# Performance work log

Hardware: AMD Instinct MI355X
Metric: run time of the kernel (lower is better)

Reference implementation:

```python
import jax, jax.numpy as jnp
import numpy as np

B, LQ, LK = 8, 64, 256
E, H, D, NH = 128, 4, 32, 128  # embed_time, num_heads, input_dim, nhidden
EK = E // H


def setup_inputs() -> dict:
    key = jax.random.key(0)
    ks = jax.random.split(key, 10)
    s = 1.0 / np.sqrt(E)
    so = 1.0 / np.sqrt(D * H)
    return {
        "query": jax.random.normal(ks[0], (B, LQ, E), jnp.float32),
        "key": jax.random.normal(ks[1], (B, LK, E), jnp.float32),
        "value": jax.random.normal(ks[2], (B, LK, D), jnp.float32),
        "mask": jax.random.randint(ks[3], (B, LK, D), 0, 2, jnp.int32),
        "Wq": jax.random.uniform(ks[4], (E, E), jnp.float32, -s, s),
        "bq": jax.random.uniform(ks[5], (E,), jnp.float32, -s, s),
        "Wk": jax.random.uniform(ks[6], (E, E), jnp.float32, -s, s),
        "bk": jax.random.uniform(ks[7], (E,), jnp.float32, -s, s),
        "Wo": jax.random.uniform(ks[8], (D * H, NH), jnp.float32, -so, so),
        "bo": jax.random.uniform(ks[9], (NH,), jnp.float32, -so, so),
    }


def reference(query, key, value, mask, Wq, bq, Wk, bk, Wo, bo):
    # project and split heads: [B, L, E] -> [B, H, L, EK]
    q = (query @ Wq + bq).reshape(B, LQ, H, EK).transpose(0, 2, 1, 3)
    k = (key @ Wk + bk).reshape(B, LK, H, EK).transpose(0, 2, 1, 3)
    # scores: [B, H, LQ, LK]
    scores = jnp.einsum("bhqe,bhke->bhqk", q, k) / jnp.sqrt(jnp.asarray(EK, q.dtype))
    # per-feature masked logits: [B, H, LQ, LK, D] (broadcast, matches repeat_interleave)
    m = mask[:, None, None, :, :]  # [B,1,1,LK,D]
    logits = jnp.where(m == 0, jnp.asarray(-1e9, q.dtype), scores[..., None])
    p = jax.nn.softmax(logits, axis=-2)  # softmax over LK, per feature channel
    # weighted sum over LK: [B, H, LQ, D]
    x = jnp.sum(p * value[:, None, None, :, :], axis=-2)
    # merge heads: [B, LQ, H*D]
    x = x.transpose(0, 2, 1, 3).reshape(B, LQ, H * D)
    return x @ Wo + bo
```

## Files before the change

### kernel.cpp

```cpp
#include <hip/hip_runtime.h>

#define B_ 8
#define LQ_ 64
#define LK_ 256
#define E_ 128
#define H_ 4
#define D_ 32
#define NH_ 128
#define EK_ 32

__global__ __launch_bounds__(512) void fused_attn_kernel(
    const float* __restrict__ query, const float* __restrict__ key,
    const float* __restrict__ value, const int* __restrict__ mask,
    const float* __restrict__ Wq, const float* __restrict__ bq,
    const float* __restrict__ Wk,
    const float* __restrict__ Wo, const float* __restrict__ bo,
    float* __restrict__ out)
{
    const int blk = blockIdx.x;
    const int b  = blk >> 5;
    const int q0 = (blk & 31) * 2;
    const int t  = threadIdx.x;

    __shared__ float e_lds[8 * LK_];
    __shared__ float smem[9472];

    float* qrow  = smem;
    float* qpart = smem + 256;
    float* qp    = smem + 768;
    float* g     = smem + 1024;
    float* spart = smem + 2048;
    float* nump  = smem;
    float* denp  = smem + 4096;
    float* x     = smem + 8192;
    float* opart = smem + 8448;

    const int d  = t & 31;
    const int kg = t >> 5;
    float vv[16], mfv[16];
    {
        const float* vb = value + ((size_t)(b * LK_) + kg * 16) * D_ + d;
        const int*   mb = mask  + ((size_t)(b * LK_) + kg * 16) * D_ + d;
        #pragma unroll
        for (int j = 0; j < 16; ++j) {
            vv[j]  = vb[j * D_];
            mfv[j] = (float)mb[j * D_];
        }
    }

    if (t < 64) {
        reinterpret_cast<float4*>(qrow)[t] =
            reinterpret_cast<const float4*>(query + ((size_t)(b * LQ_) + q0) * E_)[t];
    }
    __syncthreads();

    {
        const int col = t & 127;
        const int z   = t >> 7;
        const int r   = z & 1;
        const int eh  = z >> 1;
        const float4* qr4 = reinterpret_cast<const float4*>(qrow + r * 128 + eh * 64);
        const float* wq = Wq + (size_t)(eh * 64) * E_ + col;
        float acc = 0.0f;
        #pragma unroll
        for (int j = 0; j < 16; ++j) {
            float4 qv = qr4[j];
            acc = fmaf(qv.x, wq[(size_t)(j * 4 + 0) * E_], acc);
            acc = fmaf(qv.y, wq[(size_t)(j * 4 + 1) * E_], acc);
            acc = fmaf(qv.z, wq[(size_t)(j * 4 + 2) * E_], acc);
            acc = fmaf(qv.w, wq[(size_t)(j * 4 + 3) * E_], acc);
        }
        qpart[z * 128 + col] = acc;
    }
    __syncthreads();

    if (t < 256) {
        const int col = t & 127, r = t >> 7;
        qp[r * 128 + col] =
            qpart[r * 128 + col] + qpart[(2 + r) * 128 + col] + bq[col];
    }
    __syncthreads();

    {
        const float inv_sqrt_ek = 0.17677669529663687f;
        const int e = t >> 2;
        const int p = t & 3;
        const float4* wk4 = reinterpret_cast<const float4*>(Wk + (size_t)e * E_ + p * EK_);
        float4 w[8];
        #pragma unroll
        for (int j = 0; j < 8; ++j) w[j] = wk4[j];
        #pragma unroll
        for (int r = 0; r < 2; ++r) {
            const float4* qp4 = reinterpret_cast<const float4*>(qp + r * 128 + p * EK_);
            float acc = 0.0f;
            #pragma unroll
            for (int j = 0; j < 8; ++j) {
                float4 pv = qp4[j];
                acc = fmaf(w[j].x, pv.x, acc);
                acc = fmaf(w[j].y, pv.y, acc);
                acc = fmaf(w[j].z, pv.z, acc);
                acc = fmaf(w[j].w, pv.w, acc);
            }
            g[(r * 4 + p) * 128 + e] = acc * inv_sqrt_ek;
        }
    }
    __syncthreads();

    {
        const int k  = t & 255;
        const int eh = t >> 8;
        const float4* kr =
            reinterpret_cast<const float4*>(key + ((size_t)(b * LK_) + k) * E_ + eh * 64);
        float acc[8] = {0.f, 0.f, 0.f, 0.f, 0.f, 0.f, 0.f, 0.f};
        #pragma unroll
        for (int j = 0; j < 16; ++j) {
            float4 kv = kr[j];
            #pragma unroll
            for (int rh = 0; rh < 8; ++rh) {
                float4 gg = reinterpret_cast<const float4*>(g + rh * 128 + eh * 64)[j];
                acc[rh] = fmaf(kv.x, gg.x, acc[rh]);
                acc[rh] = fmaf(kv.y, gg.y, acc[rh]);
                acc[rh] = fmaf(kv.z, gg.z, acc[rh]);
                acc[rh] = fmaf(kv.w, gg.w, acc[rh]);
            }
        }
        #pragma unroll
        for (int rh = 0; rh < 8; ++rh)
            spart[(eh * 8 + rh) * 256 + k] = acc[rh];
    }
    __syncthreads();

    {
        const int w = t >> 6;
        const int l = t & 63;
        float4 s0 = *reinterpret_cast<const float4*>(&spart[w * 256 + l * 4]);
        float4 s1 = *reinterpret_cast<const float4*>(&spart[(8 + w) * 256 + l * 4]);
        s0.x += s1.x; s0.y += s1.y; s0.z += s1.z; s0.w += s1.w;
        float m = fmaxf(fmaxf(s0.x, s0.y), fmaxf(s0.z, s0.w));
        #pragma unroll
        for (int off = 32; off; off >>= 1)
            m = fmaxf(m, __shfl_xor(m, off));
        float4 e;
        e.x = __expf(s0.x - m); e.y = __expf(s0.y - m);
        e.z = __expf(s0.z - m); e.w = __expf(s0.w - m);
        *reinterpret_cast<float4*>(&e_lds[w * LK_ + l * 4]) = e;
    }
    __syncthreads();

    {
        float num[8] = {0.f, 0.f, 0.f, 0.f, 0.f, 0.f, 0.f, 0.f};
        float den[8] = {0.f, 0.f, 0.f, 0.f, 0.f, 0.f, 0.f, 0.f};
        #pragma unroll
        for (int jq = 0; jq < 4; ++jq) {
            const float4 mv4 = make_float4(mfv[jq*4+0]*vv[jq*4+0], mfv[jq*4+1]*vv[jq*4+1],
                                           mfv[jq*4+2]*vv[jq*4+2], mfv[jq*4+3]*vv[jq*4+3]);
            const float4 mf4 = make_float4(mfv[jq*4+0], mfv[jq*4+1],
                                           mfv[jq*4+2], mfv[jq*4+3]);
            #pragma unroll
            for (int rh = 0; rh < 8; ++rh) {
                float4 ev = *reinterpret_cast<const float4*>(
                    &e_lds[rh * LK_ + kg * 16 + jq * 4]);
                num[rh] = fmaf(ev.x, mv4.x, num[rh]);
                num[rh] = fmaf(ev.y, mv4.y, num[rh]);
                num[rh] = fmaf(ev.z, mv4.z, num[rh]);
                num[rh] = fmaf(ev.w, mv4.w, num[rh]);
                den[rh] = fmaf(ev.x, mf4.x, den[rh]);
                den[rh] = fmaf(ev.y, mf4.y, den[rh]);
                den[rh] = fmaf(ev.z, mf4.z, den[rh]);
                den[rh] = fmaf(ev.w, mf4.w, den[rh]);
            }
        }
        #pragma unroll
        for (int rh = 0; rh < 8; ++rh) {
            nump[(kg * 8 + rh) * 32 + d] = num[rh];
            denp[(kg * 8 + rh) * 32 + d] = den[rh];
        }
    }
    __syncthreads();

    if (t < 256) {
        const int rh = t >> 5, dd = t & 31;
        float n = 0.f, dn = 0.f;
        #pragma unroll
        for (int k2 = 0; k2 < 16; ++k2) {
            n  += nump[(k2 * 8 + rh) * 32 + dd];
            dn += denp[(k2 * 8 + rh) * 32 + dd];
        }
        x[(rh >> 2) * 128 + (rh & 3) * 32 + dd] = n / dn;
    }
    __syncthreads();

    {
        const int col = t & 127;
        const int eq  = t >> 7;
        const int c0  = eq * 32;
        const float* wo = Wo + (size_t)c0 * NH_ + col;
        const float4* x40 = reinterpret_cast<const float4*>(x + c0);
        const float4* x41 = reinterpret_cast<const float4*>(x + 128 + c0);
        float acc0 = 0.f, acc1 = 0.f;
        #pragma unroll
        for (int j = 0; j < 8; ++j) {
            float4 xv0 = x40[j];
            float4 xv1 = x41[j];
            float w0 = wo[(size_t)(j * 4 + 0) * NH_];
            float w1 = wo[(size_t)(j * 4 + 1) * NH_];
            float w2 = wo[(size_t)(j * 4 + 2) * NH_];
            float w3 = wo[(size_t)(j * 4 + 3) * NH_];
            acc0 = fmaf(xv0.x, w0, acc0); acc1 = fmaf(xv1.x, w0, acc1);
            acc0 = fmaf(xv0.y, w1, acc0); acc1 = fmaf(xv1.y, w1, acc1);
            acc0 = fmaf(xv0.z, w2, acc0); acc1 = fmaf(xv1.z, w2, acc1);
            acc0 = fmaf(xv0.w, w3, acc0); acc1 = fmaf(xv1.w, w3, acc1);
        }
        opart[(eq * 2 + 0) * 128 + col] = acc0;
        opart[(eq * 2 + 1) * 128 + col] = acc1;
    }
    __syncthreads();

    if (t < 256) {
        const int col = t & 127, r = t >> 7;
        float s = bo[col];
        #pragma unroll
        for (int eq = 0; eq < 4; ++eq)
            s += opart[(eq * 2 + r) * 128 + col];
        out[((size_t)(b * LQ_) + q0 + r) * NH_ + col] = s;
    }
}

extern "C" void kernel_launch(void* const* d_in, const int* in_sizes, int n_in,
                              void* d_out, int out_size, void* d_ws, size_t ws_size,
                              hipStream_t stream) {
    const float* query = (const float*)d_in[0];
    const float* key   = (const float*)d_in[1];
    const float* value = (const float*)d_in[2];
    const int*   mask  = (const int*)d_in[3];
    const float* Wq    = (const float*)d_in[4];
    const float* bq    = (const float*)d_in[5];
    const float* Wk    = (const float*)d_in[6];
    const float* Wo    = (const float*)d_in[8];
    const float* bo    = (const float*)d_in[9];
    float* out = (float*)d_out;

    fused_attn_kernel<<<B_ * (LQ_ / 2), 512, 0, stream>>>(
        query, key, value, mask, Wq, bq, Wk, Wo, bo, out);
}
```

Measured before the change: 17.26 us.

## Process one query row per block and swizzle block-to-batch mapping

Each block now handles a single query row instead of two, doubling the grid to 512 blocks. Every stage's thread mapping is reworked to match (query projection split four ways, two keys per thread in the score stage, four heads instead of eight rows). Blocks are also swizzled so consecutive block IDs span batches, and launch bounds request four blocks per CU. The aim is to fill more CUs on the device and shorten each block's critical path. The cost is that value, mask, key and weight loads are repeated per row, and only 256 threads are active in the softmax stage.

```diff
diff --git a/kernel.cpp b/kernel.cpp
--- a/kernel.cpp
+++ b/kernel.cpp
@@ -9,7 +9,7 @@
 #define NH_ 128
 #define EK_ 32
 
-__global__ __launch_bounds__(512) void fused_attn_kernel(
+__global__ __launch_bounds__(512, 4) void fused_attn_kernel(
     const float* __restrict__ query, const float* __restrict__ key,
     const float* __restrict__ value, const int* __restrict__ mask,
     const float* __restrict__ Wq, const float* __restrict__ bq,
@@ -17,23 +17,23 @@
     const float* __restrict__ Wo, const float* __restrict__ bo,
     float* __restrict__ out)
 {
-    const int blk = blockIdx.x;
-    const int b  = blk >> 5;
-    const int q0 = (blk & 31) * 2;
-    const int t  = threadIdx.x;
-
-    __shared__ float e_lds[8 * LK_];
-    __shared__ float smem[9472];
-
-    float* qrow  = smem;
-    float* qpart = smem + 256;
-    float* qp    = smem + 768;
-    float* g     = smem + 1024;
-    float* spart = smem + 2048;
+    const int blk0 = blockIdx.x;
+    const int blk  = (blk0 & 7) * 64 + (blk0 >> 3);
+    const int b = blk >> 6;
+    const int q = blk & 63;
+    const int t = threadIdx.x;
+
+    __shared__ float e_lds[4 * LK_];
+    __shared__ float smem[5248];
+
+    float* qpart = smem;
+    float* qp    = smem + 512;
+    float* g     = smem + 640;
+    float* spart = smem + 1152;
     float* nump  = smem;
-    float* denp  = smem + 4096;
-    float* x     = smem + 8192;
-    float* opart = smem + 8448;
+    float* denp  = smem + 2048;
+    float* x     = smem + 4352;
+    float* opart = smem + 4480;
 
     const int d  = t & 31;
     const int kg = t >> 5;
@@ -48,181 +48,190 @@
         }
     }
 
-    if (t < 64) {
-        reinterpret_cast<float4*>(qrow)[t] =
-            reinterpret_cast<const float4*>(query + ((size_t)(b * LQ_) + q0) * E_)[t];
-    }
-    __syncthreads();
-
     {
         const int col = t & 127;
-        const int z   = t >> 7;
-        const int r   = z & 1;
-        const int eh  = z >> 1;
-        const float4* qr4 = reinterpret_cast<const float4*>(qrow + r * 128 + eh * 64);
-        const float* wq = Wq + (size_t)(eh * 64) * E_ + col;
+        const int eq  = t >> 7;
+        const float4* qr4 = reinterpret_cast<const float4*>(
+            query + ((size_t)(b * LQ_) + q) * E_ + eq * 32);
+        const float* wq = Wq + (size_t)(eq * 32) * E_ + col;
         float acc = 0.0f;
         #pragma unroll
-        for (int j = 0; j < 16; ++j) {
+        for (int j = 0; j < 8; ++j) {
             float4 qv = qr4[j];
             acc = fmaf(qv.x, wq[(size_t)(j * 4 + 0) * E_], acc);
             acc = fmaf(qv.y, wq[(size_t)(j * 4 + 1) * E_], acc);
             acc = fmaf(qv.z, wq[(size_t)(j * 4 + 2) * E_], acc);
             acc = fmaf(qv.w, wq[(size_t)(j * 4 + 3) * E_], acc);
         }
-        qpart[z * 128 + col] = acc;
-    }
-    __syncthreads();
-
-    if (t < 256) {
-        const int col = t & 127, r = t >> 7;
-        qp[r * 128 + col] =
-            qpart[r * 128 + col] + qpart[(2 + r) * 128 + col] + bq[col];
+        qpart[eq * 128 + col] = acc;
+    }
+    __syncthreads();
+
+    if (t < 32) {
+        float4 s0 = reinterpret_cast<const float4*>(qpart)[t];
+        float4 s1 = reinterpret_cast<const float4*>(qpart)[32 + t];
+        float4 s2 = reinterpret_cast<const float4*>(qpart)[64 + t];
+        float4 s3 = reinterpret_cast<const float4*>(qpart)[96 + t];
+        float4 bv = reinterpret_cast<const float4*>(bq)[t];
+        float4 r;
+        r.x = s0.x + s1.x + s2.x + s3.x + bv.x;
+        r.y = s0.y + s1.y + s2.y + s3.y + bv.y;
+        r.z = s0.z + s1.z + s2.z + s3.z + bv.z;
+        r.w = s0.w + s1.w + s2.w + s3.w + bv.w;
+        reinterpret_cast<float4*>(qp)[t] = r;
     }
     __syncthreads();
 
     {
         const float inv_sqrt_ek = 0.17677669529663687f;
-        const int e = t >> 2;
-        const int p = t & 3;
-        const float4* wk4 = reinterpret_cast<const float4*>(Wk + (size_t)e * E_ + p * EK_);
-        float4 w[8];
-        #pragma unroll
-        for (int j = 0; j < 8; ++j) w[j] = wk4[j];
-        #pragma unroll
-        for (int r = 0; r < 2; ++r) {
-            const float4* qp4 = reinterpret_cast<const float4*>(qp + r * 128 + p * EK_);
-            float acc = 0.0f;
-            #pragma unroll
-            for (int j = 0; j < 8; ++j) {
-                float4 pv = qp4[j];
-                acc = fmaf(w[j].x, pv.x, acc);
-                acc = fmaf(w[j].y, pv.y, acc);
-                acc = fmaf(w[j].z, pv.z, acc);
-                acc = fmaf(w[j].w, pv.w, acc);
+        const int e = t & 127;
+        const int h = t >> 7;
+        const float4* wk4 =
+            reinterpret_cast<const float4*>(Wk + (size_t)e * E_ + h * EK_);
+        const float4* qp4 = reinterpret_cast<const float4*>(qp + h * EK_);
+        float acc = 0.0f;
+        #pragma unroll
+        for (int j = 0; j < 8; ++j) {
+            float4 w  = wk4[j];
+            float4 pv = qp4[j];
+            acc = fmaf(w.x, pv.x, acc);
+            acc = fmaf(w.y, pv.y, acc);
+            acc = fmaf(w.z, pv.z, acc);
+            acc = fmaf(w.w, pv.w, acc);
+        }
+        g[h * 128 + e] = acc * inv_sqrt_ek;
+    }
+    __syncthreads();
+
+    {
+        const int kq = t & 127;
+        const int ec = t >> 7;
+        const float4* kr0 = reinterpret_cast<const float4*>(
+            key + ((size_t)(b * LK_) + kq * 2 + 0) * E_ + ec * 32);
+        const float4* kr1 = reinterpret_cast<const float4*>(
+            key + ((size_t)(b * LK_) + kq * 2 + 1) * E_ + ec * 32);
+        float acc0[4] = {0.f, 0.f, 0.f, 0.f};
+        float acc1[4] = {0.f, 0.f, 0.f, 0.f};
+        #pragma unroll
+        for (int j = 0; j < 8; ++j) {
+            float4 k0 = kr0[j];
+            float4 k1 = kr1[j];
+            #pragma unroll
+            for (int h = 0; h < 4; ++h) {
+                float4 gg =
+                    reinterpret_cast<const float4*>(g + h * 128 + ec * 32)[j];
+                acc0[h] = fmaf(k0.x, gg.x, acc0[h]);
+                acc0[h] = fmaf(k0.y, gg.y, acc0[h]);
+                acc0[h] = fmaf(k0.z, gg.z, acc0[h]);
+                acc0[h] = fmaf(k0.w, gg.w, acc0[h]);
+                acc1[h] = fmaf(k1.x, gg.x, acc1[h]);
+                acc1[h] = fmaf(k1.y, gg.y, acc1[h]);
+                acc1[h] = fmaf(k1.z, gg.z, acc1[h]);
+                acc1[h] = fmaf(k1.w, gg.w, acc1[h]);
             }
-            g[(r * 4 + p) * 128 + e] = acc * inv_sqrt_ek;
-        }
-    }
-    __syncthreads();
-
-    {
-        const int k  = t & 255;
-        const int eh = t >> 8;
-        const float4* kr =
-            reinterpret_cast<const float4*>(key + ((size_t)(b * LK_) + k) * E_ + eh * 64);
-        float acc[8] = {0.f, 0.f, 0.f, 0.f, 0.f, 0.f, 0.f, 0.f};
-        #pragma unroll
-        for (int j = 0; j < 16; ++j) {
-            float4 kv = kr[j];
-            #pragma unroll
-            for (int rh = 0; rh < 8; ++rh) {
-                float4 gg = reinterpret_cast<const float4*>(g + rh * 128 + eh * 64)[j];
-                acc[rh] = fmaf(kv.x, gg.x, acc[rh]);
-                acc[rh] = fmaf(kv.y, gg.y, acc[rh]);
-                acc[rh] = fmaf(kv.z, gg.z, acc[rh]);
-                acc[rh] = fmaf(kv.w, gg.w, acc[rh]);
+        }
+        #pragma unroll
+        for (int h = 0; h < 4; ++h) {
+            *reinterpret_cast<float2*>(&spart[(ec * 4 + h) * 256 + kq * 2]) =
+                make_float2(acc0[h], acc1[h]);
+        }
+    }
+    __syncthreads();
+
+    {
+        const int w = t >> 6;
+        if (w < 4) {
+            const int h = w;
+            const int l = t & 63;
+            float4 s = *reinterpret_cast<const float4*>(
+                &spart[h * 256 + l * 4]);
+            #pragma unroll
+            for (int ec = 1; ec < 4; ++ec) {
+                float4 s2 = *reinterpret_cast<const float4*>(
+                    &spart[(ec * 4 + h) * 256 + l * 4]);
+                s.x += s2.x; s.y += s2.y; s.z += s2.z; s.w += s2.w;
             }
-        }
-        #pragma unroll
-        for (int rh = 0; rh < 8; ++rh)
-            spart[(eh * 8 + rh) * 256 + k] = acc[rh];
-    }
-    __syncthreads();
-
-    {
-        const int w = t >> 6;
-        const int l = t & 63;
-        float4 s0 = *reinterpret_cast<const float4*>(&spart[w * 256 + l * 4]);
-        float4 s1 = *reinterpret_cast<const float4*>(&spart[(8 + w) * 256 + l * 4]);
-        s0.x += s1.x; s0.y += s1.y; s0.z += s1.z; s0.w += s1.w;
-        float m = fmaxf(fmaxf(s0.x, s0.y), fmaxf(s0.z, s0.w));
-        #pragma unroll
-        for (int off = 32; off; off >>= 1)
-            m = fmaxf(m, __shfl_xor(m, off));
-        float4 e;
-        e.x = __expf(s0.x - m); e.y = __expf(s0.y - m);
-        e.z = __expf(s0.z - m); e.w = __expf(s0.w - m);
-        *reinterpret_cast<float4*>(&e_lds[w * LK_ + l * 4]) = e;
-    }
-    __syncthreads();
-
-    {
-        float num[8] = {0.f, 0.f, 0.f, 0.f, 0.f, 0.f, 0.f, 0.f};
-        float den[8] = {0.f, 0.f, 0.f, 0.f, 0.f, 0.f, 0.f, 0.f};
+            float m = fmaxf(fmaxf(s.x, s.y), fmaxf(s.z, s.w));
+            #pragma unroll
+            for (int off = 32; off; off >>= 1)
+                m = fmaxf(m, __shfl_xor(m, off));
+            float4 e4;
+            e4.x = __expf(s.x - m); e4.y = __expf(s.y - m);
+            e4.z = __expf(s.z - m); e4.w = __expf(s.w - m);
+            *reinterpret_cast<float4*>(&e_lds[h * LK_ + l * 4]) = e4;
+        }
+    }
+    __syncthreads();
+
+    {
+        float num[4] = {0.f, 0.f, 0.f, 0.f};
+        float den[4] = {0.f, 0.f, 0.f, 0.f};
         #pragma unroll
         for (int jq = 0; jq < 4; ++jq) {
-            const float4 mv4 = make_float4(mfv[jq*4+0]*vv[jq*4+0], mfv[jq*4+1]*vv[jq*4+1],
-                                           mfv[jq*4+2]*vv[jq*4+2], mfv[jq*4+3]*vv[jq*4+3]);
             const float4 mf4 = make_float4(mfv[jq*4+0], mfv[jq*4+1],
                                            mfv[jq*4+2], mfv[jq*4+3]);
-            #pragma unroll
-            for (int rh = 0; rh < 8; ++rh) {
+            const float4 mv4 = make_float4(mfv[jq*4+0]*vv[jq*4+0],
+                                           mfv[jq*4+1]*vv[jq*4+1],
+                                           mfv[jq*4+2]*vv[jq*4+2],
+                                           mfv[jq*4+3]*vv[jq*4+3]);
+            #pragma unroll
+            for (int h = 0; h < 4; ++h) {
                 float4 ev = *reinterpret_cast<const float4*>(
-                    &e_lds[rh * LK_ + kg * 16 + jq * 4]);
-                num[rh] = fmaf(ev.x, mv4.x, num[rh]);
-                num[rh] = fmaf(ev.y, mv4.y, num[rh]);
-                num[rh] = fmaf(ev.z, mv4.z, num[rh]);
-                num[rh] = fmaf(ev.w, mv4.w, num[rh]);
-                den[rh] = fmaf(ev.x, mf4.x, den[rh]);
-                den[rh] = fmaf(ev.y, mf4.y, den[rh]);
-                den[rh] = fmaf(ev.z, mf4.z, den[rh]);
-                den[rh] = fmaf(ev.w, mf4.w, den[rh]);
+                    &e_lds[h * LK_ + kg * 16 + jq * 4]);
+                num[h] = fmaf(ev.x, mv4.x, num[h]);
+                num[h] = fmaf(ev.y, mv4.y, num[h]);
+                num[h] = fmaf(ev.z, mv4.z, num[h]);
+                num[h] = fmaf(ev.w, mv4.w, num[h]);
+                den[h] = fmaf(ev.x, mf4.x, den[h]);
+                den[h] = fmaf(ev.y, mf4.y, den[h]);
+                den[h] = fmaf(ev.z, mf4.z, den[h]);
+                den[h] = fmaf(ev.w, mf4.w, den[h]);
             }
         }
         #pragma unroll
-        for (int rh = 0; rh < 8; ++rh) {
-            nump[(kg * 8 + rh) * 32 + d] = num[rh];
-            denp[(kg * 8 + rh) * 32 + d] = den[rh];
-        }
-    }
-    __syncthreads();
-
-    if (t < 256) {
-        const int rh = t >> 5, dd = t & 31;
+        for (int h = 0; h < 4; ++h) {
+            nump[(kg * 4 + h) * 32 + d] = num[h];
+            denp[(kg * 4 + h) * 32 + d] = den[h];
+        }
+    }
+    __syncthreads();
+
+    if (t < 128) {
+        const int h = t >> 5, dd = t & 31;
         float n = 0.f, dn = 0.f;
         #pragma unroll
         for (int k2 = 0; k2 < 16; ++k2) {
-            n  += nump[(k2 * 8 + rh) * 32 + dd];
-            dn += denp[(k2 * 8 + rh) * 32 + dd];
-        }
-        x[(rh >> 2) * 128 + (rh & 3) * 32 + dd] = n / dn;
+            n  += nump[(k2 * 4 + h) * 32 + dd];
+            dn += denp[(k2 * 4 + h) * 32 + dd];
+        }
+        x[h * 32 + dd] = n / dn;
     }
     __syncthreads();
 
     {
         const int col = t & 127;
-        const int eq  = t >> 7;
-        const int c0  = eq * 32;
-        const float* wo = Wo + (size_t)c0 * NH_ + col;
-        const float4* x40 = reinterpret_cast<const float4*>(x + c0);
-        const float4* x41 = reinterpret_cast<const float4*>(x + 128 + c0);
-        float acc0 = 0.f, acc1 = 0.f;
-        #pragma unroll
-        for (int j = 0; j < 8; ++j) {
-            float4 xv0 = x40[j];
-            float4 xv1 = x41[j];
-            float w0 = wo[(size_t)(j * 4 + 0) * NH_];
-            float w1 = wo[(size_t)(j * 4 + 1) * NH_];
-            float w2 = wo[(size_t)(j * 4 + 2) * NH_];
-            float w3 = wo[(size_t)(j * 4 + 3) * NH_];
-            acc0 = fmaf(xv0.x, w0, acc0); acc1 = fmaf(xv1.x, w0, acc1);
-            acc0 = fmaf(xv0.y, w1, acc0); acc1 = fmaf(xv1.y, w1, acc1);
-            acc0 = fmaf(xv0.z, w2, acc0); acc1 = fmaf(xv1.z, w2, acc1);
-            acc0 = fmaf(xv0.w, w3, acc0); acc1 = fmaf(xv1.w, w3, acc1);
-        }
-        opart[(eq * 2 + 0) * 128 + col] = acc0;
-        opart[(eq * 2 + 1) * 128 + col] = acc1;
-    }
-    __syncthreads();
-
-    if (t < 256) {
-        const int col = t & 127, r = t >> 7;
-        float s = bo[col];
-        #pragma unroll
-        for (int eq = 0; eq < 4; ++eq)
-            s += opart[(eq * 2 + r) * 128 + col];
-        out[((size_t)(b * LQ_) + q0 + r) * NH_ + col] = s;
+        const int dq  = t >> 7;
+        const float* wo = Wo + (size_t)(dq * 32) * NH_ + col;
+        const float4* x4 = reinterpret_cast<const float4*>(x + dq * 32);
+        float acc = 0.0f;
+        #pragma unroll
+        for (int j = 0; j < 8; ++j) {
+            float4 xv = x4[j];
+            acc = fmaf(xv.x, wo[(size_t)(j * 4 + 0) * NH_], acc);
+            acc = fmaf(xv.y, wo[(size_t)(j * 4 + 1) * NH_], acc);
+            acc = fmaf(xv.z, wo[(size_t)(j * 4 + 2) * NH_], acc);
+            acc = fmaf(xv.w, wo[(size_t)(j * 4 + 3) * NH_], acc);
+        }
+        opart[dq * 128 + col] = acc;
+    }
+    __syncthreads();
+
+    if (t < 128) {
+        float s = bo[t];
+        #pragma unroll
+        for (int dq = 0; dq < 4; ++dq)
+            s += opart[dq * 128 + t];
+        out[((size_t)(b * LQ_) + q) * NH_ + t] = s;
     }
 }
 
@@ -240,6 +249,6 @@
     const float* bo    = (const float*)d_in[9];
     float* out = (float*)d_out;
 
-    fused_attn_kernel<<<B_ * (LQ_ / 2), 512, 0, stream>>>(
+    fused_attn_kernel<<<B_ * LQ_, 512, 0, stream>>>(
         query, key, value, mask, Wq, bq, Wk, Wo, bo, out);
 }
```

New measurement: 25.88 us. +49.9%, slower.

## Double block size to 1024 threads and split each stage's reductions finer

Applied to the files above, without the earlier changes.

Raises the workgroup from 512 to 1024 threads and reworks every stage so each thread handles half the work: Q projection, key-score, and output projection are split into 4 partial sums instead of 2, and the value/mask accumulation covers 8 keys per thread. The partial num/den sums are combined across wave halves with a shuffle before going to shared memory. The aim is more parallelism per block to cut per-thread serial latency, since only 256 blocks run. The cost is more partial-sum reduction work, a larger shared buffer, idle threads in the softmax stage, and a tighter register budget from the 1024-thread launch bound.

```diff
diff --git a/kernel.cpp b/kernel.cpp
--- a/kernel.cpp
+++ b/kernel.cpp
@@ -9,7 +9,7 @@
 #define NH_ 128
 #define EK_ 32
 
-__global__ __launch_bounds__(512) void fused_attn_kernel(
+__global__ __launch_bounds__(1024, 4) void fused_attn_kernel(
     const float* __restrict__ query, const float* __restrict__ key,
     const float* __restrict__ value, const int* __restrict__ mask,
     const float* __restrict__ Wq, const float* __restrict__ bq,
@@ -23,13 +23,13 @@
     const int t  = threadIdx.x;
 
     __shared__ float e_lds[8 * LK_];
-    __shared__ float smem[9472];
+    __shared__ float smem[10752];
 
     float* qrow  = smem;
     float* qpart = smem + 256;
-    float* qp    = smem + 768;
-    float* g     = smem + 1024;
-    float* spart = smem + 2048;
+    float* qp    = smem + 1280;
+    float* g     = smem + 1536;
+    float* spart = smem + 2560;
     float* nump  = smem;
     float* denp  = smem + 4096;
     float* x     = smem + 8192;
@@ -37,12 +37,12 @@
 
     const int d  = t & 31;
     const int kg = t >> 5;
-    float vv[16], mfv[16];
-    {
-        const float* vb = value + ((size_t)(b * LK_) + kg * 16) * D_ + d;
-        const int*   mb = mask  + ((size_t)(b * LK_) + kg * 16) * D_ + d;
-        #pragma unroll
-        for (int j = 0; j < 16; ++j) {
+    float vv[8], mfv[8];
+    {
+        const float* vb = value + ((size_t)(b * LK_) + kg * 8) * D_ + d;
+        const int*   mb = mask  + ((size_t)(b * LK_) + kg * 8) * D_ + d;
+        #pragma unroll
+        for (int j = 0; j < 8; ++j) {
             vv[j]  = vb[j * D_];
             mfv[j] = (float)mb[j * D_];
         }
@@ -58,12 +58,12 @@
         const int col = t & 127;
         const int z   = t >> 7;
         const int r   = z & 1;
-        const int eh  = z >> 1;
-        const float4* qr4 = reinterpret_cast<const float4*>(qrow + r * 128 + eh * 64);
-        const float* wq = Wq + (size_t)(eh * 64) * E_ + col;
+        const int c4  = z >> 1;
+        const float4* qr4 = reinterpret_cast<const float4*>(qrow + r * 128 + c4 * 32);
+        const float* wq = Wq + (size_t)(c4 * 32) * E_ + col;
         float acc = 0.0f;
         #pragma unroll
-        for (int j = 0; j < 16; ++j) {
+        for (int j = 0; j < 8; ++j) {
             float4 qv = qr4[j];
             acc = fmaf(qv.x, wq[(size_t)(j * 4 + 0) * E_], acc);
             acc = fmaf(qv.y, wq[(size_t)(j * 4 + 1) * E_], acc);
@@ -76,48 +76,47 @@
 
     if (t < 256) {
         const int col = t & 127, r = t >> 7;
-        qp[r * 128 + col] =
-            qpart[r * 128 + col] + qpart[(2 + r) * 128 + col] + bq[col];
+        float s = bq[col];
+        #pragma unroll
+        for (int c4 = 0; c4 < 4; ++c4)
+            s += qpart[(c4 * 2 + r) * 128 + col];
+        qp[r * 128 + col] = s;
     }
     __syncthreads();
 
     {
         const float inv_sqrt_ek = 0.17677669529663687f;
-        const int e = t >> 2;
-        const int p = t & 3;
-        const float4* wk4 = reinterpret_cast<const float4*>(Wk + (size_t)e * E_ + p * EK_);
-        float4 w[8];
-        #pragma unroll
-        for (int j = 0; j < 8; ++j) w[j] = wk4[j];
-        #pragma unroll
-        for (int r = 0; r < 2; ++r) {
-            const float4* qp4 = reinterpret_cast<const float4*>(qp + r * 128 + p * EK_);
-            float acc = 0.0f;
-            #pragma unroll
-            for (int j = 0; j < 8; ++j) {
-                float4 pv = qp4[j];
-                acc = fmaf(w[j].x, pv.x, acc);
-                acc = fmaf(w[j].y, pv.y, acc);
-                acc = fmaf(w[j].z, pv.z, acc);
-                acc = fmaf(w[j].w, pv.w, acc);
-            }
-            g[(r * 4 + p) * 128 + e] = acc * inv_sqrt_ek;
-        }
+        const int r = t & 1;
+        const int h = (t >> 1) & 3;
+        const int e = t >> 3;
+        const float4* wk4 = reinterpret_cast<const float4*>(Wk + (size_t)e * E_ + h * EK_);
+        const float4* qp4 = reinterpret_cast<const float4*>(qp + r * 128 + h * EK_);
+        float acc = 0.0f;
+        #pragma unroll
+        for (int j = 0; j < 8; ++j) {
+            float4 w  = wk4[j];
+            float4 pv = qp4[j];
+            acc = fmaf(w.x, pv.x, acc);
+            acc = fmaf(w.y, pv.y, acc);
+            acc = fmaf(w.z, pv.z, acc);
+            acc = fmaf(w.w, pv.w, acc);
+        }
+        g[(r * 4 + h) * 128 + e] = acc * inv_sqrt_ek;
     }
     __syncthreads();
 
     {
         const int k  = t & 255;
-        const int eh = t >> 8;
+        const int zc = t >> 8;
         const float4* kr =
-            reinterpret_cast<const float4*>(key + ((size_t)(b * LK_) + k) * E_ + eh * 64);
+            reinterpret_cast<const float4*>(key + ((size_t)(b * LK_) + k) * E_ + zc * 32);
         float acc[8] = {0.f, 0.f, 0.f, 0.f, 0.f, 0.f, 0.f, 0.f};
         #pragma unroll
-        for (int j = 0; j < 16; ++j) {
+        for (int j = 0; j < 8; ++j) {
             float4 kv = kr[j];
             #pragma unroll
             for (int rh = 0; rh < 8; ++rh) {
-                float4 gg = reinterpret_cast<const float4*>(g + rh * 128 + eh * 64)[j];
+                float4 gg = reinterpret_cast<const float4*>(g + rh * 128 + zc * 32)[j];
                 acc[rh] = fmaf(kv.x, gg.x, acc[rh]);
                 acc[rh] = fmaf(kv.y, gg.y, acc[rh]);
                 acc[rh] = fmaf(kv.z, gg.z, acc[rh]);
@@ -126,24 +125,30 @@
         }
         #pragma unroll
         for (int rh = 0; rh < 8; ++rh)
-            spart[(eh * 8 + rh) * 256 + k] = acc[rh];
+            spart[(zc * 8 + rh) * 256 + k] = acc[rh];
     }
     __syncthreads();
 
     {
         const int w = t >> 6;
-        const int l = t & 63;
-        float4 s0 = *reinterpret_cast<const float4*>(&spart[w * 256 + l * 4]);
-        float4 s1 = *reinterpret_cast<const float4*>(&spart[(8 + w) * 256 + l * 4]);
-        s0.x += s1.x; s0.y += s1.y; s0.z += s1.z; s0.w += s1.w;
-        float m = fmaxf(fmaxf(s0.x, s0.y), fmaxf(s0.z, s0.w));
-        #pragma unroll
-        for (int off = 32; off; off >>= 1)
-            m = fmaxf(m, __shfl_xor(m, off));
-        float4 e;
-        e.x = __expf(s0.x - m); e.y = __expf(s0.y - m);
-        e.z = __expf(s0.z - m); e.w = __expf(s0.w - m);
-        *reinterpret_cast<float4*>(&e_lds[w * LK_ + l * 4]) = e;
+        if (w < 8) {
+            const int l = t & 63;
+            float4 s = *reinterpret_cast<const float4*>(&spart[w * 256 + l * 4]);
+            #pragma unroll
+            for (int zc = 1; zc < 4; ++zc) {
+                float4 s2 = *reinterpret_cast<const float4*>(
+                    &spart[(zc * 8 + w) * 256 + l * 4]);
+                s.x += s2.x; s.y += s2.y; s.z += s2.z; s.w += s2.w;
+            }
+            float m = fmaxf(fmaxf(s.x, s.y), fmaxf(s.z, s.w));
+            #pragma unroll
+            for (int off = 32; off; off >>= 1)
+                m = fmaxf(m, __shfl_xor(m, off));
+            float4 e4;
+            e4.x = __expf(s.x - m); e4.y = __expf(s.y - m);
+            e4.z = __expf(s.z - m); e4.w = __expf(s.w - m);
+            *reinterpret_cast<float4*>(&e_lds[w * LK_ + l * 4]) = e4;
+        }
     }
     __syncthreads();
 
@@ -151,15 +156,17 @@
         float num[8] = {0.f, 0.f, 0.f, 0.f, 0.f, 0.f, 0.f, 0.f};
         float den[8] = {0.f, 0.f, 0.f, 0.f, 0.f, 0.f, 0.f, 0.f};
         #pragma unroll
-        for (int jq = 0; jq < 4; ++jq) {
-            const float4 mv4 = make_float4(mfv[jq*4+0]*vv[jq*4+0], mfv[jq*4+1]*vv[jq*4+1],
-                                           mfv[jq*4+2]*vv[jq*4+2], mfv[jq*4+3]*vv[jq*4+3]);
+        for (int jq = 0; jq < 2; ++jq) {
             const float4 mf4 = make_float4(mfv[jq*4+0], mfv[jq*4+1],
                                            mfv[jq*4+2], mfv[jq*4+3]);
+            const float4 mv4 = make_float4(mfv[jq*4+0]*vv[jq*4+0],
+                                           mfv[jq*4+1]*vv[jq*4+1],
+                                           mfv[jq*4+2]*vv[jq*4+2],
+                                           mfv[jq*4+3]*vv[jq*4+3]);
             #pragma unroll
             for (int rh = 0; rh < 8; ++rh) {
                 float4 ev = *reinterpret_cast<const float4*>(
-                    &e_lds[rh * LK_ + kg * 16 + jq * 4]);
+                    &e_lds[rh * LK_ + kg * 8 + jq * 4]);
                 num[rh] = fmaf(ev.x, mv4.x, num[rh]);
                 num[rh] = fmaf(ev.y, mv4.y, num[rh]);
                 num[rh] = fmaf(ev.z, mv4.z, num[rh]);
@@ -172,8 +179,16 @@
         }
         #pragma unroll
         for (int rh = 0; rh < 8; ++rh) {
-            nump[(kg * 8 + rh) * 32 + d] = num[rh];
-            denp[(kg * 8 + rh) * 32 + d] = den[rh];
+            num[rh] += __shfl_xor(num[rh], 32);
+            den[rh] += __shfl_xor(den[rh], 32);
+        }
+        if ((kg & 1) == 0) {
+            const int kgp = kg >> 1;
+            #pragma unroll
+            for (int rh = 0; rh < 8; ++rh) {
+                nump[(kgp * 8 + rh) * 32 + d] = num[rh];
+                denp[(kgp * 8 + rh) * 32 + d] = den[rh];
+            }
         }
     }
     __syncthreads();
@@ -192,27 +207,21 @@
 
     {
         const int col = t & 127;
-        const int eq  = t >> 7;
-        const int c0  = eq * 32;
-        const float* wo = Wo + (size_t)c0 * NH_ + col;
-        const float4* x40 = reinterpret_cast<const float4*>(x + c0);
-        const float4* x41 = reinterpret_cast<const float4*>(x + 128 + c0);
-        float acc0 = 0.f, acc1 = 0.f;
-        #pragma unroll
-        for (int j = 0; j < 8; ++j) {
-            float4 xv0 = x40[j];
-            float4 xv1 = x41[j];
-            float w0 = wo[(size_t)(j * 4 + 0) * NH_];
-            float w1 = wo[(size_t)(j * 4 + 1) * NH_];
-            float w2 = wo[(size_t)(j * 4 + 2) * NH_];
-            float w3 = wo[(size_t)(j * 4 + 3) * NH_];
-            acc0 = fmaf(xv0.x, w0, acc0); acc1 = fmaf(xv1.x, w0, acc1);
-            acc0 = fmaf(xv0.y, w1, acc0); acc1 = fmaf(xv1.y, w1, acc1);
-            acc0 = fmaf(xv0.z, w2, acc0); acc1 = fmaf(xv1.z, w2, acc1);
-            acc0 = fmaf(xv0.w, w3, acc0); acc1 = fmaf(xv1.w, w3, acc1);
-        }
-        opart[(eq * 2 + 0) * 128 + col] = acc0;
-        opart[(eq * 2 + 1) * 128 + col] = acc1;
+        const int z   = t >> 7;
+        const int r   = z & 1;
+        const int dq  = z >> 1;
+        const float* wo = Wo + (size_t)(dq * 32) * NH_ + col;
+        const float4* x4 = reinterpret_cast<const float4*>(x + r * 128 + dq * 32);
+        float acc = 0.0f;
+        #pragma unroll
+        for (int j = 0; j < 8; ++j) {
+            float4 xv = x4[j];
+            acc = fmaf(xv.x, wo[(size_t)(j * 4 + 0) * NH_], acc);
+            acc = fmaf(xv.y, wo[(size_t)(j * 4 + 1) * NH_], acc);
+            acc = fmaf(xv.z, wo[(size_t)(j * 4 + 2) * NH_], acc);
+            acc = fmaf(xv.w, wo[(size_t)(j * 4 + 3) * NH_], acc);
+        }
+        opart[(dq * 2 + r) * 128 + col] = acc;
     }
     __syncthreads();
 
@@ -220,8 +229,8 @@
         const int col = t & 127, r = t >> 7;
         float s = bo[col];
         #pragma unroll
-        for (int eq = 0; eq < 4; ++eq)
-            s += opart[(eq * 2 + r) * 128 + col];
+        for (int dq = 0; dq < 4; ++dq)
+            s += opart[(dq * 2 + r) * 128 + col];
         out[((size_t)(b * LQ_) + q0 + r) * NH_ + col] = s;
     }
 }
@@ -240,6 +249,6 @@
     const float* bo    = (const float*)d_in[9];
     float* out = (float*)d_out;
 
-    fused_attn_kernel<<<B_ * (LQ_ / 2), 512, 0, stream>>>(
+    fused_attn_kernel<<<B_ * (LQ_ / 2), 1024, 0, stream>>>(
         query, key, value, mask, Wq, bq, Wk, Wo, bo, out);
 }
```

Measured after the change: 18.49 us. +7.1%, slower.

## Prefetch weights, keys, values and mask into registers ahead of dependent stages

Applied to the files above, without the earlier changes.

Moves the global loads of Wk rows, biases, key rows, value and mask ahead of the earlier projection stages so their latency overlaps the Q-projection and reductions instead of stalling each stage. It also replaces two __syncthreads with a raw s_waitcnt lgkmcnt(0)+s_barrier that does not wait on outstanding global loads, and sets launch_bounds to 512 with min 2 blocks per CU. The trade-off is much higher register pressure (kreg 64 floats, wkr 32, vv/mfv 32), which could force spills under the tighter occupancy bound.

```diff
diff --git a/kernel.cpp b/kernel.cpp
--- a/kernel.cpp
+++ b/kernel.cpp
@@ -9,7 +9,10 @@
 #define NH_ 128
 #define EK_ 32
 
-__global__ __launch_bounds__(512) void fused_attn_kernel(
+
+#define RAW_BARRIER() asm volatile("s_waitcnt lgkmcnt(0)\n\ts_barrier" ::: "memory")
+
+__global__ __launch_bounds__(512, 2) void fused_attn_kernel(
     const float* __restrict__ query, const float* __restrict__ key,
     const float* __restrict__ value, const int* __restrict__ mask,
     const float* __restrict__ Wq, const float* __restrict__ bq,
@@ -35,22 +38,25 @@
     float* x     = smem + 8192;
     float* opart = smem + 8448;
 
-    const int d  = t & 31;
-    const int kg = t >> 5;
-    float vv[16], mfv[16];
-    {
-        const float* vb = value + ((size_t)(b * LK_) + kg * 16) * D_ + d;
-        const int*   mb = mask  + ((size_t)(b * LK_) + kg * 16) * D_ + d;
-        #pragma unroll
-        for (int j = 0; j < 16; ++j) {
-            vv[j]  = vb[j * D_];
-            mfv[j] = (float)mb[j * D_];
-        }
+    float4 qv0;
+    if (t < 64)
+        qv0 = reinterpret_cast<const float4*>(query + ((size_t)(b * LQ_) + q0) * E_)[t];
+    float bqv = 0.0f, bov = 0.0f;
+    if (t < 256) {
+        bqv = bq[t & 127];
+        bov = bo[t & 127];
+    }
+    const int e4 = t >> 2, p4 = t & 3;
+    float4 wkr[8];
+    {
+        const float4* wk4 =
+            reinterpret_cast<const float4*>(Wk + (size_t)e4 * E_ + p4 * EK_);
+        #pragma unroll
+        for (int j = 0; j < 8; ++j) wkr[j] = wk4[j];
     }
 
     if (t < 64) {
-        reinterpret_cast<float4*>(qrow)[t] =
-            reinterpret_cast<const float4*>(query + ((size_t)(b * LQ_) + q0) * E_)[t];
+        reinterpret_cast<float4*>(qrow)[t] = qv0;
     }
     __syncthreads();
 
@@ -74,50 +80,61 @@
     }
     __syncthreads();
 
+    const int k5 = t & 255, eh5 = t >> 8;
+    float4 kreg[16];
+    {
+        const float4* kr = reinterpret_cast<const float4*>(
+            key + ((size_t)(b * LK_) + k5) * E_ + eh5 * 64);
+        #pragma unroll
+        for (int j = 0; j < 16; ++j) kreg[j] = kr[j];
+    }
+    const int d  = t & 31;
+    const int kg = t >> 5;
+    float vv[16], mfv[16];
+    {
+        const float* vb = value + ((size_t)(b * LK_) + kg * 16) * D_ + d;
+        const int*   mb = mask  + ((size_t)(b * LK_) + kg * 16) * D_ + d;
+        #pragma unroll
+        for (int j = 0; j < 16; ++j) {
+            vv[j]  = vb[j * D_];
+            mfv[j] = (float)mb[j * D_];
+        }
+    }
+
     if (t < 256) {
         const int col = t & 127, r = t >> 7;
         qp[r * 128 + col] =
-            qpart[r * 128 + col] + qpart[(2 + r) * 128 + col] + bq[col];
-    }
-    __syncthreads();
+            qpart[r * 128 + col] + qpart[(2 + r) * 128 + col] + bqv;
+    }
+    RAW_BARRIER();
 
     {
         const float inv_sqrt_ek = 0.17677669529663687f;
-        const int e = t >> 2;
-        const int p = t & 3;
-        const float4* wk4 = reinterpret_cast<const float4*>(Wk + (size_t)e * E_ + p * EK_);
-        float4 w[8];
-        #pragma unroll
-        for (int j = 0; j < 8; ++j) w[j] = wk4[j];
         #pragma unroll
         for (int r = 0; r < 2; ++r) {
-            const float4* qp4 = reinterpret_cast<const float4*>(qp + r * 128 + p * EK_);
+            const float4* qp4 = reinterpret_cast<const float4*>(qp + r * 128 + p4 * EK_);
             float acc = 0.0f;
             #pragma unroll
             for (int j = 0; j < 8; ++j) {
                 float4 pv = qp4[j];
-                acc = fmaf(w[j].x, pv.x, acc);
-                acc = fmaf(w[j].y, pv.y, acc);
-                acc = fmaf(w[j].z, pv.z, acc);
-                acc = fmaf(w[j].w, pv.w, acc);
+                acc = fmaf(wkr[j].x, pv.x, acc);
+                acc = fmaf(wkr[j].y, pv.y, acc);
+                acc = fmaf(wkr[j].z, pv.z, acc);
+                acc = fmaf(wkr[j].w, pv.w, acc);
             }
-            g[(r * 4 + p) * 128 + e] = acc * inv_sqrt_ek;
-        }
-    }
-    __syncthreads();
-
-    {
-        const int k  = t & 255;
-        const int eh = t >> 8;
-        const float4* kr =
-            reinterpret_cast<const float4*>(key + ((size_t)(b * LK_) + k) * E_ + eh * 64);
+            g[(r * 4 + p4) * 128 + e4] = acc * inv_sqrt_ek;
+        }
+    }
+    RAW_BARRIER();
+
+    {
         float acc[8] = {0.f, 0.f, 0.f, 0.f, 0.f, 0.f, 0.f, 0.f};
         #pragma unroll
         for (int j = 0; j < 16; ++j) {
-            float4 kv = kr[j];
+            float4 kv = kreg[j];
             #pragma unroll
             for (int rh = 0; rh < 8; ++rh) {
-                float4 gg = reinterpret_cast<const float4*>(g + rh * 128 + eh * 64)[j];
+                float4 gg = reinterpret_cast<const float4*>(g + rh * 128 + eh5 * 64)[j];
                 acc[rh] = fmaf(kv.x, gg.x, acc[rh]);
                 acc[rh] = fmaf(kv.y, gg.y, acc[rh]);
                 acc[rh] = fmaf(kv.z, gg.z, acc[rh]);
@@ -126,7 +143,7 @@
         }
         #pragma unroll
         for (int rh = 0; rh < 8; ++rh)
-            spart[(eh * 8 + rh) * 256 + k] = acc[rh];
+            spart[(eh5 * 8 + rh) * 256 + k5] = acc[rh];
     }
     __syncthreads();
 
@@ -218,7 +235,7 @@
 
     if (t < 256) {
         const int col = t & 127, r = t >> 7;
-        float s = bo[col];
+        float s = bov;
         #pragma unroll
         for (int eq = 0; eq < 4; ++eq)
             s += opart[(eq * 2 + r) * 128 + col];
```

Measured after the change: 18.31 us. 6.1% more time.
